# Performance work log

Hardware: AMD Instinct MI355X
Metric: run time of the kernel (lower is better)

Reference implementation:

```python
import jax, jax.numpy as jnp
import numpy as np
from jax import lax

N, S, C, D1, D2, P = 16384, 4096, 3, 256, 256, 16
MLP = [256, 256]
IN_CH = D1 + D2
K = 3
BIG = 1e8
EPS = 1e-8
BN_EPS = 1e-5


def setup_inputs() -> dict:
    key = jax.random.key(0)
    ks = jax.random.split(key, 16)
    inp = {
        'xyz1': jax.random.normal(ks[0], (1, C, N), jnp.float32),
        'xyz2': jax.random.normal(ks[1], (1, C, S), jnp.float32),
        'piece_id1': jax.random.randint(ks[2], (1, 1, N), 0, P, jnp.int64),
        'piece_id2': jax.random.randint(ks[3], (1, 1, S), 0, P, jnp.int64),
        'points1': jax.random.normal(ks[4], (1, D1, N), jnp.float32),
        'points2': jax.random.normal(ks[5], (1, D2, S), jnp.float32),
    }
    last = IN_CH
    for i, out in enumerate(MLP):
        inp[f'w{i}'] = jax.random.normal(ks[6 + 2 * i], (out, last), jnp.float32) / np.sqrt(last)
        inp[f'b{i}'] = jnp.zeros((out,), jnp.float32)
        inp[f'g{i}'] = jnp.ones((out,), jnp.float32)
        inp[f'bt{i}'] = jnp.zeros((out,), jnp.float32)
        last = out
    return inp


def _interpolate(xyz1, xyz2, pid1, pid2, points2):
    # xyz1 [1,3,N], xyz2 [1,3,S], pid [1,1,N]/[1,1,S], points2 [1,D,S]
    p1 = xyz1[0].T          # [N,3]
    p2 = xyz2[0].T          # [S,3]
    id1 = pid1[0, 0]        # [N]
    id2 = pid2[0, 0]        # [S]
    # squared euclidean distances, masked to same-piece neighbors (knn with batch vectors)
    d = jnp.sum((p1[:, None, :] - p2[None, :, :]) ** 2, axis=-1)  # [N,S]
    d = jnp.where(id1[:, None] != id2[None, :], jnp.inf, d)
    neg_d3, idx = lax.top_k(-d, K)    # 3 nearest per query
    d3 = -neg_d3                      # [N,3]
    valid = jnp.isfinite(d3)
    # missing neighbors -> reuse first idx with huge distance (fill_value semantics)
    idx = jnp.where(valid, idx, idx[:, :1])
    d3 = jnp.where(valid, d3, BIG)
    w = 1.0 / (d3 + EPS)
    w = w / jnp.sum(w, axis=-1, keepdims=True)   # [N,3]
    f2 = points2[0].T                            # [S,D2]
    interp = jnp.sum(f2[idx] * w[..., None], axis=1)  # [N,D2]
    return interp


def reference(xyz1, xyz2, piece_id1, piece_id2, points1, points2,
              w0, b0, g0, bt0, w1, b1, g1, bt1):
    interp = _interpolate(xyz1, xyz2, piece_id1, piece_id2, points2)  # [N,D2]
    feats = jnp.concatenate([points1[0].T, interp], axis=-1)          # [N,Cin]
    x = feats.T[None]                                                  # [1,Cin,N]
    for (wc, bc, g, bt) in ((w0, b0, g0, bt0), (w1, b1, g1, bt1)):
        y = jnp.einsum('oc,bcn->bon', wc, x) + bc[None, :, None]
        mean = jnp.mean(y, axis=(0, 2), keepdims=True)
        var = jnp.mean((y - mean) ** 2, axis=(0, 2), keepdims=True)
        y = (y - mean) * lax.rsqrt(var + BN_EPS)
        y = y * g[None, :, None] + bt[None, :, None]
        x = jax.nn.relu(y)
    return x
```

## Files before the change

kernel.cpp:

```cpp
#include <hip/hip_runtime.h>
#include <math.h>

#define NQ 16384
#define NS 4096
#define NCH 256
#define NP 16
#define BIGD 1e8f
#define EPSW 1e-8f

typedef __attribute__((ext_vector_type(8))) short short8;
typedef __attribute__((ext_vector_type(4))) float f32x4;

static __device__ __forceinline__ unsigned short f2bf(float x) {
    unsigned u = __float_as_uint(x);
    unsigned r = (u + 0x7fff + ((u >> 16) & 1)) >> 16;
    return (unsigned short)r;
}
static __device__ __forceinline__ float bf2f(unsigned short u) {
    return __uint_as_float(((unsigned)u) << 16);
}

__global__ __launch_bounds__(1024)
void bucket_kernel(const float* __restrict__ xyz2, const int* __restrict__ pid2,
                   float4* __restrict__ bpts, int* __restrict__ boff)
{
    __shared__ int spid[NS];
    __shared__ int segcnt[64][NP];
    __shared__ int segbase[64][NP];
    __shared__ int poff[NP + 1];
    const int t = threadIdx.x;
    for (int i = t; i < NS; i += 1024) spid[i] = pid2[i];
    __syncthreads();
    {
        const int seg = t >> 4, p = t & 15;
        int c = 0;
        const int b = seg * 64;
        for (int i = 0; i < 64; ++i) c += (spid[b + i] == p);
        segcnt[seg][p] = c;
    }
    __syncthreads();
    if (t < NP) {
        int run = 0;
        for (int s = 0; s < 64; ++s) { segbase[s][t] = run; run += segcnt[s][t]; }
        poff[t] = run;
    }
    __syncthreads();
    if (t == 0) {
        int run = 0;
        for (int p = 0; p < NP; ++p) { int c = poff[p]; poff[p] = run; run += c; }
        poff[NP] = run;
    }
    __syncthreads();
    if (t <= NP) boff[t] = poff[t];
    {
        const int seg = t >> 4, p = t & 15;
        int pos = poff[p] + segbase[seg][p];
        const int b = seg * 64;
        for (int i = 0; i < 64; ++i) {
            const int gi = b + i;
            if (spid[gi] == p) {
                bpts[pos] = make_float4(xyz2[gi], xyz2[NS + gi], xyz2[2 * NS + gi],
                                        __int_as_float(gi));
                ++pos;
            }
        }
    }
}

#define LEXLT(d, j, e, je) ((d) < (e) || ((d) == (e) && (j) < (je)))

__global__ __launch_bounds__(256)
void knn_kernel(const float* __restrict__ xyz1, const int* __restrict__ pid1,
                const float4* __restrict__ bpts, const int* __restrict__ boff,
                int* __restrict__ oidx, float* __restrict__ ow)
{
    const int t = blockIdx.x * 256 + threadIdx.x;
    const int q = t >> 4;
    const int k = t & 15;
    const float qx = xyz1[q], qy = xyz1[NQ + q], qz = xyz1[2 * NQ + q];
    const int p = pid1[q];
    const int s0 = boff[p], s1 = boff[p + 1];

    float e0 = INFINITY, e1 = INFINITY, e2 = INFINITY;
    int j0 = 0, j1 = 0, j2 = 0;
    for (int i = s0 + k; i < s1; i += 16) {
        float4 pt = bpts[i];
        const float dx = pt.x - qx, dy = pt.y - qy, dz = pt.z - qz;
        const float d = fmaf(dx, dx, fmaf(dy, dy, dz * dz));
        const int oi = __float_as_int(pt.w);
        const bool b0 = LEXLT(d, oi, e0, j0), b1 = LEXLT(d, oi, e1, j1),
                   b2 = LEXLT(d, oi, e2, j2);
        e2 = b2 ? (b1 ? e1 : d) : e2;  j2 = b2 ? (b1 ? j1 : oi) : j2;
        e1 = b1 ? (b0 ? e0 : d) : e1;  j1 = b1 ? (b0 ? j0 : oi) : j1;
        e0 = b0 ? d : e0;              j0 = b0 ? oi : j0;
    }
    #pragma unroll
    for (int m = 1; m <= 8; m <<= 1) {
        float f[3]; int gi[3];
        f[0] = __shfl_xor(e0, m); gi[0] = __shfl_xor(j0, m);
        f[1] = __shfl_xor(e1, m); gi[1] = __shfl_xor(j1, m);
        f[2] = __shfl_xor(e2, m); gi[2] = __shfl_xor(j2, m);
        #pragma unroll
        for (int c = 0; c < 3; ++c) {
            const float d = f[c]; const int oi = gi[c];
            const bool b0 = LEXLT(d, oi, e0, j0), b1 = LEXLT(d, oi, e1, j1),
                       b2 = LEXLT(d, oi, e2, j2);
            e2 = b2 ? (b1 ? e1 : d) : e2;  j2 = b2 ? (b1 ? j1 : oi) : j2;
            e1 = b1 ? (b0 ? e0 : d) : e1;  j1 = b1 ? (b0 ? j0 : oi) : j1;
            e0 = b0 ? d : e0;              j0 = b0 ? oi : j0;
        }
    }
    if (k == 0) {
        if (isinf(e0)) { j0 = 0;  e0 = BIGD; }
        if (isinf(e1)) { j1 = j0; e1 = BIGD; }
        if (isinf(e2)) { j2 = j0; e2 = BIGD; }
        const float w0 = 1.f / (e0 + EPSW), w1 = 1.f / (e1 + EPSW), w2 = 1.f / (e2 + EPSW);
        const float inv = 1.f / (w0 + w1 + w2);
        oidx[q * 3 + 0] = j0; oidx[q * 3 + 1] = j1; oidx[q * 3 + 2] = j2;
        ow[q * 3 + 0] = w0 * inv; ow[q * 3 + 1] = w1 * inv; ow[q * 3 + 2] = w2 * inv;
    }
}

__global__ __launch_bounds__(256)
void cvtw_kernel(const float* __restrict__ w0, const float* __restrict__ w1,
                 unsigned short* __restrict__ o0, unsigned short* __restrict__ o1)
{
    const int i = blockIdx.x * 256 + threadIdx.x;
    const float* src; unsigned short* dst; int j;
    if (i < 32768) { src = w0; dst = o0; j = i; }
    else           { src = w1; dst = o1; j = i - 32768; }
    float4 v = ((const float4*)src)[j];
    ushort4 o;
    o.x = f2bf(v.x); o.y = f2bf(v.y); o.z = f2bf(v.z); o.w = f2bf(v.w);
    ((ushort4*)dst)[j] = o;
}

__global__ __launch_bounds__(256)
void tcvt_kernel(const float* __restrict__ src, int srcN,
                 unsigned short* __restrict__ dst, int kt, int coff)
{
    __shared__ float tile[64][65];
    const int cb = blockIdx.x * 64;
    const int nb = blockIdx.y * 64;
    #pragma unroll
    for (int rnd = 0; rnd < 4; ++rnd) {
        const int r = rnd * 16 + (threadIdx.x >> 4);
        const int c4 = (threadIdx.x & 15) * 4;
        float4 v = *(const float4*)&src[(size_t)(cb + r) * srcN + nb + c4];
        tile[r][c4 + 0] = v.x; tile[r][c4 + 1] = v.y;
        tile[r][c4 + 2] = v.z; tile[r][c4 + 3] = v.w;
    }
    __syncthreads();
    #pragma unroll
    for (int half = 0; half < 2; ++half) {
        const int p  = (threadIdx.x >> 3) + half * 32;
        const int cg = threadIdx.x & 7;
        ushort4 o0, o1;
        o0.x = f2bf(tile[cg * 8 + 0][p]); o0.y = f2bf(tile[cg * 8 + 1][p]);
        o0.z = f2bf(tile[cg * 8 + 2][p]); o0.w = f2bf(tile[cg * 8 + 3][p]);
        o1.x = f2bf(tile[cg * 8 + 4][p]); o1.y = f2bf(tile[cg * 8 + 5][p]);
        o1.z = f2bf(tile[cg * 8 + 6][p]); o1.w = f2bf(tile[cg * 8 + 7][p]);
        ushort4* d = (ushort4*)&dst[(size_t)(nb + p) * kt + coff + cb + cg * 8];
        d[0] = o0; d[1] = o1;
    }
}

__global__ __launch_bounds__(256)
void interp_kernel(const unsigned short* __restrict__ p2Tb,
                   const int* __restrict__ oidx, const float* __restrict__ ow,
                   unsigned short* __restrict__ Xt)
{
    const int n = (blockIdx.x * 256 + threadIdx.x) >> 6;
    const int l = threadIdx.x & 63;
    const int i0 = oidx[n * 3 + 0], i1 = oidx[n * 3 + 1], i2 = oidx[n * 3 + 2];
    const float w0 = ow[n * 3 + 0], w1 = ow[n * 3 + 1], w2 = ow[n * 3 + 2];
    ushort4 a = *(const ushort4*)&p2Tb[(size_t)i0 * 256 + l * 4];
    ushort4 b = *(const ushort4*)&p2Tb[(size_t)i1 * 256 + l * 4];
    ushort4 c = *(const ushort4*)&p2Tb[(size_t)i2 * 256 + l * 4];
    ushort4 o;
    o.x = f2bf(w0 * bf2f(a.x) + w1 * bf2f(b.x) + w2 * bf2f(c.x));
    o.y = f2bf(w0 * bf2f(a.y) + w1 * bf2f(b.y) + w2 * bf2f(c.y));
    o.z = f2bf(w0 * bf2f(a.z) + w1 * bf2f(b.z) + w2 * bf2f(c.z));
    o.w = f2bf(w0 * bf2f(a.w) + w1 * bf2f(b.w) + w2 * bf2f(c.w));
    *(ushort4*)&Xt[(size_t)n * 512 + 256 + l * 4] = o;
}

template<int K, bool LOAD_DIRECT>
__global__ __launch_bounds__(512)
void mgemm_kernel(const unsigned short* __restrict__ Wb,
                  const unsigned short* __restrict__ Xsrc,
                  const float* __restrict__ sum_in, const float* __restrict__ sq_in,
                  const float* __restrict__ g, const float* __restrict__ bt,
                  unsigned short* __restrict__ Yout)
{
    constexpr int K2 = K * 2;
    __shared__ unsigned char sB[32 * K2];
    const int tid = threadIdx.x;
    const int n0 = blockIdx.x * 32;

    if constexpr (!LOAD_DIRECT) {
        __shared__ float scs[256], shs[256];
        if (tid < 256) {
            const float mean = sum_in[tid] * (1.f / NQ);
            const float var  = sq_in[tid] * (1.f / NQ) - mean * mean;
            const float rs = rsqrtf(var + 1e-5f);
            const float s = g[tid] * rs;
            scs[tid] = s; shs[tid] = bt[tid] - mean * s;
        }
        __syncthreads();
        const int row = tid >> 4;
        #pragma unroll
        for (int ch = 0; ch < 2; ++ch) {
            const int cb = (tid & 15) * 32 + ch * 16;
            const int c = cb / 2;
            const short8 v = *(const short8*)&Xsrc[(size_t)(n0 + row) * 256 + c];
            ushort4 lo, hi;
            lo.x = f2bf(fmaxf(fmaf(bf2f((unsigned short)v[0]), scs[c+0], shs[c+0]), 0.f));
            lo.y = f2bf(fmaxf(fmaf(bf2f((unsigned short)v[1]), scs[c+1], shs[c+1]), 0.f));
            lo.z = f2bf(fmaxf(fmaf(bf2f((unsigned short)v[2]), scs[c+2], shs[c+2]), 0.f));
            lo.w = f2bf(fmaxf(fmaf(bf2f((unsigned short)v[3]), scs[c+3], shs[c+3]), 0.f));
            hi.x = f2bf(fmaxf(fmaf(bf2f((unsigned short)v[4]), scs[c+4], shs[c+4]), 0.f));
            hi.y = f2bf(fmaxf(fmaf(bf2f((unsigned short)v[5]), scs[c+5], shs[c+5]), 0.f));
            hi.z = f2bf(fmaxf(fmaf(bf2f((unsigned short)v[6]), scs[c+6], shs[c+6]), 0.f));
            hi.w = f2bf(fmaxf(fmaf(bf2f((unsigned short)v[7]), scs[c+7], shs[c+7]), 0.f));
            unsigned char* d = &sB[row * K2 + (cb ^ ((row & 7) << 4))];
            ((ushort4*)d)[0] = lo; ((ushort4*)d)[1] = hi;
        }
    } else {
        constexpr int ROUNDS = (32 * K2 / 16) / 512;
        #pragma unroll
        for (int j = 0; j < ROUNDS; ++j) {
            const int p   = (j * 512 + tid) * 16;
            const int row = p >> 10;
            const int c   = p & (K2 - 1);
            const int q   = c ^ ((row & 7) << 4);
            const char* gp = (const char*)(Xsrc + (size_t)(n0 + row) * K) + q;
            __builtin_amdgcn_global_load_lds(
                (const __attribute__((address_space(1))) void*)gp,
                (__attribute__((address_space(3))) void*)(sB + p), 16, 0, 0);
        }
    }
    __syncthreads();

    const int w = tid >> 6, l = tid & 63;
    const int lr = l & 15, lk = l >> 4;
    const int mbase = w * 32;
    f32x4 acc[2][2] = {};
    #pragma unroll
    for (int ks = 0; ks < K / 32; ++ks) {
        short8 b[2];
        #pragma unroll
        for (int nf = 0; nf < 2; ++nf) {
            const int r = nf * 16 + lr;
            const int cbyte = ks * 64 + lk * 16;
            b[nf] = *(const short8*)&sB[r * K2 + (cbyte ^ ((r & 7) << 4))];
        }
        #pragma unroll
        for (int mf = 0; mf < 2; ++mf) {
            const int m = mbase + mf * 16 + lr;
            const short8 a = *(const short8*)&Wb[(size_t)m * K + ks * 32 + lk * 8];
            #pragma unroll
            for (int nf = 0; nf < 2; ++nf)
                acc[mf][nf] = __builtin_amdgcn_mfma_f32_16x16x32_bf16(
                                  a, b[nf], acc[mf][nf], 0, 0, 0);
        }
    }
    #pragma unroll
    for (int mf = 0; mf < 2; ++mf)
        #pragma unroll
        for (int nf = 0; nf < 2; ++nf) {
            const int n = n0 + nf * 16 + lr;
            const int moff = mbase + mf * 16 + lk * 4;
            ushort4 o;
            o.x = f2bf(acc[mf][nf][0]); o.y = f2bf(acc[mf][nf][1]);
            o.z = f2bf(acc[mf][nf][2]); o.w = f2bf(acc[mf][nf][3]);
            *(ushort4*)&Yout[(size_t)n * 256 + moff] = o;
        }
}

__global__ __launch_bounds__(256)
void stats_kernel(const unsigned short* __restrict__ Y,
                  float* __restrict__ sum, float* __restrict__ sq)
{
    __shared__ float red[2][8][256];
    const int t = threadIdx.x;
    const int c8 = (t & 31) * 8;
    const int rsub = t >> 5;
    const int r0 = blockIdx.x * 512 + rsub;
    float s[8] = {}, q[8] = {};
    for (int i = 0; i < 64; ++i) {
        const short8 v = *(const short8*)&Y[(size_t)(r0 + i * 8) * 256 + c8];
        #pragma unroll
        for (int j = 0; j < 8; ++j) {
            const float f = bf2f((unsigned short)v[j]);
            s[j] += f; q[j] += f * f;
        }
    }
    #pragma unroll
    for (int j = 0; j < 8; ++j) {
        red[0][rsub][c8 + j] = s[j];
        red[1][rsub][c8 + j] = q[j];
    }
    __syncthreads();
    float ts = 0.f, tq = 0.f;
    #pragma unroll
    for (int r = 0; r < 8; ++r) { ts += red[0][r][t]; tq += red[1][r][t]; }
    atomicAdd(&sum[t], ts);
    atomicAdd(&sq[t], tq);
}

__global__ __launch_bounds__(256)
void bnt_kernel(const unsigned short* __restrict__ Y, const float* __restrict__ sum,
                const float* __restrict__ sq, const float* __restrict__ g,
                const float* __restrict__ bt, float* __restrict__ out)
{
    __shared__ float tile[64][65];
    __shared__ float scs[64], shs[64];
    const int t = threadIdx.x;
    const int cb = blockIdx.x * 64;
    const int nb = blockIdx.y * 64;
    if (t < 64) {
        const int c = cb + t;
        const float mean = sum[c] * (1.f / NQ);
        const float var  = sq[c] * (1.f / NQ) - mean * mean;
        const float rs = rsqrtf(var + 1e-5f);
        const float s = g[c] * rs;
        scs[t] = s; shs[t] = bt[c] - mean * s;
    }
    __syncthreads();
    #pragma unroll
    for (int rnd = 0; rnd < 4; ++rnd) {
        const int nl = rnd * 16 + (t >> 4);
        const int c4 = (t & 15) * 4;
        ushort4 v = *(const ushort4*)&Y[(size_t)(nb + nl) * 256 + cb + c4];
        tile[c4 + 0][nl] = fmaxf(fmaf(bf2f(v.x), scs[c4 + 0], shs[c4 + 0]), 0.f);
        tile[c4 + 1][nl] = fmaxf(fmaf(bf2f(v.y), scs[c4 + 1], shs[c4 + 1]), 0.f);
        tile[c4 + 2][nl] = fmaxf(fmaf(bf2f(v.z), scs[c4 + 2], shs[c4 + 2]), 0.f);
        tile[c4 + 3][nl] = fmaxf(fmaf(bf2f(v.w), scs[c4 + 3], shs[c4 + 3]), 0.f);
    }
    __syncthreads();
    const int cl = t >> 2, qq = t & 3;
    float* orow = out + (size_t)(cb + cl) * NQ + nb + qq * 16;
    #pragma unroll
    for (int k = 0; k < 4; ++k) {
        float4 v = make_float4(tile[cl][qq * 16 + k * 4 + 0], tile[cl][qq * 16 + k * 4 + 1],
                               tile[cl][qq * 16 + k * 4 + 2], tile[cl][qq * 16 + k * 4 + 3]);
        *(float4*)&orow[k * 4] = v;
    }
}

extern "C" void kernel_launch(void* const* d_in, const int* in_sizes, int n_in,
                              void* d_out, int out_size, void* d_ws, size_t ws_size,
                              hipStream_t stream)
{
    const float* xyz1    = (const float*)d_in[0];
    const float* xyz2    = (const float*)d_in[1];
    const int*   pid1    = (const int*)d_in[2];
    const int*   pid2    = (const int*)d_in[3];
    const float* points1 = (const float*)d_in[4];
    const float* points2 = (const float*)d_in[5];
    const float* w0      = (const float*)d_in[6];
    const float* g0      = (const float*)d_in[8];
    const float* bt0     = (const float*)d_in[9];
    const float* w1      = (const float*)d_in[10];
    const float* g1      = (const float*)d_in[12];
    const float* bt1     = (const float*)d_in[13];
    float* out = (float*)d_out;

    char* ws = (char*)d_ws;
    int*            boff  = (int*)(ws + 0);
    float*          sums  = (float*)(ws + 128);
    float*          sum0  = sums, *sq0 = sums + 256, *sum1 = sums + 512, *sq1 = sums + 768;
    int*            idxb  = (int*)(ws + 8192);
    float*          wb    = (float*)(ws + 8192 + 196608);
    unsigned short* Wb0   = (unsigned short*)(ws + 8192 + 393216);
    unsigned short* Wb1   = (unsigned short*)(ws + 8192 + 655360);
    float4*         bpts  = (float4*)(ws + 8192 + 786432);
    unsigned short* p2Tb  = (unsigned short*)(ws + 1048576);
    unsigned short* Xt    = (unsigned short*)(ws + 1048576 + 2097152);
    unsigned short* y0Tb  = (unsigned short*)(ws + 1048576 + 2097152 + 16777216);
    unsigned short* y1Tb  = (unsigned short*)(ws + 1048576 + 2097152 + 25165824);

    hipMemsetAsync(sums, 0, 4096, stream);
    bucket_kernel<<<1, 1024, 0, stream>>>(xyz2, pid2, bpts, boff);
    knn_kernel<<<NQ * 16 / 256, 256, 0, stream>>>(xyz1, pid1, bpts, boff, idxb, wb);
    cvtw_kernel<<<192, 256, 0, stream>>>(w0, w1, Wb0, Wb1);
    tcvt_kernel<<<dim3(4, NS / 64), 256, 0, stream>>>(points2, NS, p2Tb, 256, 0);
    tcvt_kernel<<<dim3(4, NQ / 64), 256, 0, stream>>>(points1, NQ, Xt, 512, 0);
    interp_kernel<<<NQ * 64 / 256, 256, 0, stream>>>(p2Tb, idxb, wb, Xt);
    mgemm_kernel<512, true><<<NQ / 32, 512, 0, stream>>>(
        Wb0, Xt, nullptr, nullptr, nullptr, nullptr, y0Tb);
    stats_kernel<<<32, 256, 0, stream>>>(y0Tb, sum0, sq0);
    mgemm_kernel<256, false><<<NQ / 32, 512, 0, stream>>>(
        Wb1, y0Tb, sum0, sq0, g0, bt0, y1Tb);
    stats_kernel<<<32, 256, 0, stream>>>(y1Tb, sum1, sq1);
    bnt_kernel<<<dim3(4, NQ / 64), 256, 0, stream>>>(y1Tb, sum1, sq1, g1, bt1, out);
}
```

Baseline: 200.4 us.

## Fuse prep conversions, pre-swizzle weights into MFMA fragment order, widen stats grid

Merges the weight conversion and both transpose-convert kernels into one prep kernel. It also folds the stats memset into bucket_kernel, which cuts launch count and overhead. Weights are now stored in MFMA fragment order, so each lane's A-operand load in the GEMM reads a contiguous 16-byte chunk instead of a strided row. The BN scale/shift loads use float4 LDS reads, and the stats kernel doubles its grid to 64 blocks for more parallelism, at the cost of more atomics. The sums zeroing now relies on bucket_kernel running with 1024 threads covering all 1024 floats.

```diff
diff --git a/kernel.cpp b/kernel.cpp
--- a/kernel.cpp
+++ b/kernel.cpp
@@ -22,13 +22,15 @@
 
 __global__ __launch_bounds__(1024)
 void bucket_kernel(const float* __restrict__ xyz2, const int* __restrict__ pid2,
-                   float4* __restrict__ bpts, int* __restrict__ boff)
+                   float4* __restrict__ bpts, int* __restrict__ boff,
+                   float* __restrict__ sums)
 {
     __shared__ int spid[NS];
     __shared__ int segcnt[64][NP];
     __shared__ int segbase[64][NP];
     __shared__ int poff[NP + 1];
     const int t = threadIdx.x;
+    sums[t] = 0.f;
     for (int i = t; i < NS; i += 1024) spid[i] = pid2[i];
     __syncthreads();
     {
@@ -121,31 +123,16 @@
     }
 }
 
-__global__ __launch_bounds__(256)
-void cvtw_kernel(const float* __restrict__ w0, const float* __restrict__ w1,
-                 unsigned short* __restrict__ o0, unsigned short* __restrict__ o1)
-{
-    const int i = blockIdx.x * 256 + threadIdx.x;
-    const float* src; unsigned short* dst; int j;
-    if (i < 32768) { src = w0; dst = o0; j = i; }
-    else           { src = w1; dst = o1; j = i - 32768; }
-    float4 v = ((const float4*)src)[j];
-    ushort4 o;
-    o.x = f2bf(v.x); o.y = f2bf(v.y); o.z = f2bf(v.z); o.w = f2bf(v.w);
-    ((ushort4*)dst)[j] = o;
-}
-
-__global__ __launch_bounds__(256)
-void tcvt_kernel(const float* __restrict__ src, int srcN,
-                 unsigned short* __restrict__ dst, int kt, int coff)
-{
-    __shared__ float tile[64][65];
-    const int cb = blockIdx.x * 64;
-    const int nb = blockIdx.y * 64;
+static __device__ __forceinline__
+void tcvt_body(const float* __restrict__ src, int srcN,
+               unsigned short* __restrict__ dst, int kt,
+               int cb, int nb, float (*tile)[65])
+{
+    const int t = threadIdx.x;
     #pragma unroll
     for (int rnd = 0; rnd < 4; ++rnd) {
-        const int r = rnd * 16 + (threadIdx.x >> 4);
-        const int c4 = (threadIdx.x & 15) * 4;
+        const int r = rnd * 16 + (t >> 4);
+        const int c4 = (t & 15) * 4;
         float4 v = *(const float4*)&src[(size_t)(cb + r) * srcN + nb + c4];
         tile[r][c4 + 0] = v.x; tile[r][c4 + 1] = v.y;
         tile[r][c4 + 2] = v.z; tile[r][c4 + 3] = v.w;
@@ -153,15 +140,53 @@
     __syncthreads();
     #pragma unroll
     for (int half = 0; half < 2; ++half) {
-        const int p  = (threadIdx.x >> 3) + half * 32;
-        const int cg = threadIdx.x & 7;
+        const int p  = (t >> 3) + half * 32;
+        const int cg = t & 7;
         ushort4 o0, o1;
         o0.x = f2bf(tile[cg * 8 + 0][p]); o0.y = f2bf(tile[cg * 8 + 1][p]);
         o0.z = f2bf(tile[cg * 8 + 2][p]); o0.w = f2bf(tile[cg * 8 + 3][p]);
         o1.x = f2bf(tile[cg * 8 + 4][p]); o1.y = f2bf(tile[cg * 8 + 5][p]);
         o1.z = f2bf(tile[cg * 8 + 6][p]); o1.w = f2bf(tile[cg * 8 + 7][p]);
-        ushort4* d = (ushort4*)&dst[(size_t)(nb + p) * kt + coff + cb + cg * 8];
+        ushort4* d = (ushort4*)&dst[(size_t)(nb + p) * kt + cb + cg * 8];
         d[0] = o0; d[1] = o1;
+    }
+}
+
+static __device__ __forceinline__
+void wrelay_body(const float* __restrict__ src, unsigned short* __restrict__ dst,
+                 int K, int kslog, int o4)
+{
+    const int e4 = o4 & 1;
+    const int tmp = o4 >> 1;
+    const int l = tmp & 63;
+    const int gks = tmp >> 6;
+    const int ks = gks & ((1 << kslog) - 1);
+    const int g  = gks >> kslog;
+    const int row = g * 16 + (l & 15);
+    const int col = ks * 32 + (l >> 4) * 8 + e4 * 4;
+    float4 v = *(const float4*)&src[(size_t)row * K + col];
+    ushort4 o;
+    o.x = f2bf(v.x); o.y = f2bf(v.y); o.z = f2bf(v.z); o.w = f2bf(v.w);
+    ((ushort4*)dst)[o4] = o;
+}
+
+__global__ __launch_bounds__(256)
+void prep_kernel(const float* __restrict__ points1, const float* __restrict__ points2,
+                 const float* __restrict__ w0, const float* __restrict__ w1,
+                 unsigned short* __restrict__ Xt, unsigned short* __restrict__ p2Tb,
+                 unsigned short* __restrict__ Wf0, unsigned short* __restrict__ Wf1)
+{
+    __shared__ float tile[64][65];
+    const int b = blockIdx.x;
+    if (b < 1024) {
+        tcvt_body(points1, NQ, Xt, 512, (b & 3) * 64, (b >> 2) * 64, tile);
+    } else if (b < 1280) {
+        const int bb = b - 1024;
+        tcvt_body(points2, NS, p2Tb, 256, (bb & 3) * 64, (bb >> 2) * 64, tile);
+    } else if (b < 1408) {
+        wrelay_body(w0, Wf0, 512, 4, (b - 1280) * 256 + threadIdx.x);
+    } else {
+        wrelay_body(w1, Wf1, 256, 3, (b - 1408) * 256 + threadIdx.x);
     }
 }
 
@@ -187,13 +212,14 @@
 
 template<int K, bool LOAD_DIRECT>
 __global__ __launch_bounds__(512)
-void mgemm_kernel(const unsigned short* __restrict__ Wb,
+void mgemm_kernel(const unsigned short* __restrict__ Wf,
                   const unsigned short* __restrict__ Xsrc,
                   const float* __restrict__ sum_in, const float* __restrict__ sq_in,
                   const float* __restrict__ g, const float* __restrict__ bt,
                   unsigned short* __restrict__ Yout)
 {
     constexpr int K2 = K * 2;
+    constexpr int KS = K / 32;
     __shared__ unsigned char sB[32 * K2];
     const int tid = threadIdx.x;
     const int n0 = blockIdx.x * 32;
@@ -214,15 +240,17 @@
             const int cb = (tid & 15) * 32 + ch * 16;
             const int c = cb / 2;
             const short8 v = *(const short8*)&Xsrc[(size_t)(n0 + row) * 256 + c];
+            const float4 s0 = *(const float4*)&scs[c],     s1 = *(const float4*)&scs[c + 4];
+            const float4 h0 = *(const float4*)&shs[c],     h1 = *(const float4*)&shs[c + 4];
             ushort4 lo, hi;
-            lo.x = f2bf(fmaxf(fmaf(bf2f((unsigned short)v[0]), scs[c+0], shs[c+0]), 0.f));
-            lo.y = f2bf(fmaxf(fmaf(bf2f((unsigned short)v[1]), scs[c+1], shs[c+1]), 0.f));
-            lo.z = f2bf(fmaxf(fmaf(bf2f((unsigned short)v[2]), scs[c+2], shs[c+2]), 0.f));
-            lo.w = f2bf(fmaxf(fmaf(bf2f((unsigned short)v[3]), scs[c+3], shs[c+3]), 0.f));
-            hi.x = f2bf(fmaxf(fmaf(bf2f((unsigned short)v[4]), scs[c+4], shs[c+4]), 0.f));
-            hi.y = f2bf(fmaxf(fmaf(bf2f((unsigned short)v[5]), scs[c+5], shs[c+5]), 0.f));
-            hi.z = f2bf(fmaxf(fmaf(bf2f((unsigned short)v[6]), scs[c+6], shs[c+6]), 0.f));
-            hi.w = f2bf(fmaxf(fmaf(bf2f((unsigned short)v[7]), scs[c+7], shs[c+7]), 0.f));
+            lo.x = f2bf(fmaxf(fmaf(bf2f((unsigned short)v[0]), s0.x, h0.x), 0.f));
+            lo.y = f2bf(fmaxf(fmaf(bf2f((unsigned short)v[1]), s0.y, h0.y), 0.f));
+            lo.z = f2bf(fmaxf(fmaf(bf2f((unsigned short)v[2]), s0.z, h0.z), 0.f));
+            lo.w = f2bf(fmaxf(fmaf(bf2f((unsigned short)v[3]), s0.w, h0.w), 0.f));
+            hi.x = f2bf(fmaxf(fmaf(bf2f((unsigned short)v[4]), s1.x, h1.x), 0.f));
+            hi.y = f2bf(fmaxf(fmaf(bf2f((unsigned short)v[5]), s1.y, h1.y), 0.f));
+            hi.z = f2bf(fmaxf(fmaf(bf2f((unsigned short)v[6]), s1.z, h1.z), 0.f));
+            hi.w = f2bf(fmaxf(fmaf(bf2f((unsigned short)v[7]), s1.w, h1.w), 0.f));
             unsigned char* d = &sB[row * K2 + (cb ^ ((row & 7) << 4))];
             ((ushort4*)d)[0] = lo; ((ushort4*)d)[1] = hi;
         }
@@ -244,10 +272,9 @@
 
     const int w = tid >> 6, l = tid & 63;
     const int lr = l & 15, lk = l >> 4;
-    const int mbase = w * 32;
     f32x4 acc[2][2] = {};
     #pragma unroll
-    for (int ks = 0; ks < K / 32; ++ks) {
+    for (int ks = 0; ks < KS; ++ks) {
         short8 b[2];
         #pragma unroll
         for (int nf = 0; nf < 2; ++nf) {
@@ -257,8 +284,8 @@
         }
         #pragma unroll
         for (int mf = 0; mf < 2; ++mf) {
-            const int m = mbase + mf * 16 + lr;
-            const short8 a = *(const short8*)&Wb[(size_t)m * K + ks * 32 + lk * 8];
+            const short8 a = *(const short8*)(
+                Wf + (((size_t)(w * 2 + mf) * KS + ks) * 64 + l) * 8);
             #pragma unroll
             for (int nf = 0; nf < 2; ++nf)
                 acc[mf][nf] = __builtin_amdgcn_mfma_f32_16x16x32_bf16(
@@ -270,7 +297,7 @@
         #pragma unroll
         for (int nf = 0; nf < 2; ++nf) {
             const int n = n0 + nf * 16 + lr;
-            const int moff = mbase + mf * 16 + lk * 4;
+            const int moff = w * 32 + mf * 16 + lk * 4;
             ushort4 o;
             o.x = f2bf(acc[mf][nf][0]); o.y = f2bf(acc[mf][nf][1]);
             o.z = f2bf(acc[mf][nf][2]); o.w = f2bf(acc[mf][nf][3]);
@@ -286,9 +313,9 @@
     const int t = threadIdx.x;
     const int c8 = (t & 31) * 8;
     const int rsub = t >> 5;
-    const int r0 = blockIdx.x * 512 + rsub;
+    const int r0 = blockIdx.x * 256 + rsub;
     float s[8] = {}, q[8] = {};
-    for (int i = 0; i < 64; ++i) {
+    for (int i = 0; i < 32; ++i) {
         const short8 v = *(const short8*)&Y[(size_t)(r0 + i * 8) * 256 + c8];
         #pragma unroll
         for (int j = 0; j < 8; ++j) {
@@ -373,26 +400,23 @@
     float*          sum0  = sums, *sq0 = sums + 256, *sum1 = sums + 512, *sq1 = sums + 768;
     int*            idxb  = (int*)(ws + 8192);
     float*          wb    = (float*)(ws + 8192 + 196608);
-    unsigned short* Wb0   = (unsigned short*)(ws + 8192 + 393216);
-    unsigned short* Wb1   = (unsigned short*)(ws + 8192 + 655360);
+    unsigned short* Wf0   = (unsigned short*)(ws + 8192 + 393216);
+    unsigned short* Wf1   = (unsigned short*)(ws + 8192 + 655360);
     float4*         bpts  = (float4*)(ws + 8192 + 786432);
     unsigned short* p2Tb  = (unsigned short*)(ws + 1048576);
     unsigned short* Xt    = (unsigned short*)(ws + 1048576 + 2097152);
     unsigned short* y0Tb  = (unsigned short*)(ws + 1048576 + 2097152 + 16777216);
     unsigned short* y1Tb  = (unsigned short*)(ws + 1048576 + 2097152 + 25165824);
 
-    hipMemsetAsync(sums, 0, 4096, stream);
-    bucket_kernel<<<1, 1024, 0, stream>>>(xyz2, pid2, bpts, boff);
+    bucket_kernel<<<1, 1024, 0, stream>>>(xyz2, pid2, bpts, boff, sums);
     knn_kernel<<<NQ * 16 / 256, 256, 0, stream>>>(xyz1, pid1, bpts, boff, idxb, wb);
-    cvtw_kernel<<<192, 256, 0, stream>>>(w0, w1, Wb0, Wb1);
-    tcvt_kernel<<<dim3(4, NS / 64), 256, 0, stream>>>(points2, NS, p2Tb, 256, 0);
-    tcvt_kernel<<<dim3(4, NQ / 64), 256, 0, stream>>>(points1, NQ, Xt, 512, 0);
+    prep_kernel<<<1472, 256, 0, stream>>>(points1, points2, w0, w1, Xt, p2Tb, Wf0, Wf1);
     interp_kernel<<<NQ * 64 / 256, 256, 0, stream>>>(p2Tb, idxb, wb, Xt);
     mgemm_kernel<512, true><<<NQ / 32, 512, 0, stream>>>(
-        Wb0, Xt, nullptr, nullptr, nullptr, nullptr, y0Tb);
-    stats_kernel<<<32, 256, 0, stream>>>(y0Tb, sum0, sq0);
+        Wf0, Xt, nullptr, nullptr, nullptr, nullptr, y0Tb);
+    stats_kernel<<<64, 256, 0, stream>>>(y0Tb, sum0, sq0);
     mgemm_kernel<256, false><<<NQ / 32, 512, 0, stream>>>(
-        Wb1, y0Tb, sum0, sq0, g0, bt0, y1Tb);
-    stats_kernel<<<32, 256, 0, stream>>>(y1Tb, sum1, sq1);
+        Wf1, y0Tb, sum0, sq0, g0, bt0, y1Tb);
+    stats_kernel<<<64, 256, 0, stream>>>(y1Tb, sum1, sq1);
     bnt_kernel<<<dim3(4, NQ / 64), 256, 0, stream>>>(y1Tb, sum1, sq1, g1, bt1, out);
 }
```

Result: faster. 176.5 us (-12.0%).
